# Performance work log

Measured on AMD Instinct MI355X. Metric: run time of the kernel, lower is better.

## Reference

```python
import jax, jax.numpy as jnp
import numpy as np

EPS = 0.1        # entropic regularization (init eps)
MAX_ITER = 100   # init max_iter
THRESH = 0.1     # early-stop threshold from original code
NORM_EPS = 1e-8


def setup_inputs() -> dict:
    key = jax.random.key(0)
    kx, ky = jax.random.split(key)
    x = jax.random.normal(kx, (16, 1024, 256), dtype=jnp.float32)
    y = jax.random.normal(ky, (16, 1024, 256), dtype=jnp.float32)
    return {"x": x, "y": y}


def _mfa_cost(x, y):
    # Cosine cost: E = 1 - cos(x_i, y_j), computed via normalized matmul
    # (norms clamped at 1e-8 as in torch CosineSimilarity).
    xn = x / jnp.maximum(jnp.linalg.norm(x, axis=-1, keepdims=True), NORM_EPS)
    yn = y / jnp.maximum(jnp.linalg.norm(y, axis=-1, keepdims=True), NORM_EPS)
    E = 1.0 - jnp.einsum('bnd,bmd->bnm', xn, yn)  # [B, N, M]

    B, N, M = E.shape
    log_mu = jnp.full((B, N), jnp.log(1.0 / N + 1e-8), dtype=E.dtype)
    log_nu = jnp.full((B, M), jnp.log(1.0 / M + 1e-8), dtype=E.dtype)

    def Mmat(u, v):
        # (-E + u_i + v_j) / eps, broadcast over [B, N, M]
        return (-E + u[..., :, None] + v[..., None, :]) / EPS

    @jax.checkpoint
    def body(carry, _):
        u, v, done = carry
        u_new = EPS * (log_mu - jax.nn.logsumexp(Mmat(u, v), axis=-1)) + u
        # original transposes then logsumexp over -1 == logsumexp over -2
        v_new = EPS * (log_nu - jax.nn.logsumexp(Mmat(u_new, v), axis=-2)) + v
        err = jnp.abs(u_new - u).sum(-1).mean()
        # emulate data-dependent break: freeze u, v once converged
        u_out = jnp.where(done, u, u_new)
        v_out = jnp.where(done, v, v_new)
        return (u_out, v_out, done | (err < THRESH)), None

    u0 = jnp.zeros((B, N), dtype=E.dtype)
    v0 = jnp.zeros((B, M), dtype=E.dtype)
    (u, v, _), _ = jax.lax.scan(body, (u0, v0, jnp.array(False)), None, length=MAX_ITER)

    pi = jnp.exp(Mmat(u, v))                 # transport plan [B, N, M]
    cost = jnp.sum(pi * E, axis=(-2, -1))    # [B]  (reduction='none')
    return cost


def reference(x, y):
    return _mfa_cost(x, y)
```

## Files before the change

### kernel.cpp

```cpp
#include <hip/hip_runtime.h>

typedef _Float16 half_t;
typedef __attribute__((ext_vector_type(8))) _Float16 half8;
typedef __attribute__((ext_vector_type(4))) float f32x4;
typedef __attribute__((ext_vector_type(8))) short short8v;
typedef unsigned short u16;
typedef unsigned int u32;

#define SCALE_F     14.4269504f
#define INV_SCALE_F 0.0693147181f
#define C_MU       -9.99998523f
#define C_NU       -9.99998523f
#define MU_F        0.000976572498f
#define ERR_STOP_B  1.44269504f
#define MAX_ITER    100
#define SPIN_LIMIT  50000000LL
#define PV0         3.0517578125e-05f

#define SMEM_E   131072
#define SMEM_CP  16384
#define SMEM_PV  4096
#define SMEM_RED 256
#define SMEM_TOTAL (SMEM_E + SMEM_CP + SMEM_PV + SMEM_RED)

#define PSTRIDE  520
#define NFLAGS   2048

__device__ __forceinline__ float fexp2(float x) { return __builtin_amdgcn_exp2f(x); }
__device__ __forceinline__ float flog2(float x) { return __builtin_amdgcn_logf(x); }
__device__ __forceinline__ float frcp(float x)  { return __builtin_amdgcn_rcpf(x); }

__device__ __forceinline__ u16 f2bf(float f) {
  unsigned u = __float_as_uint(f);
  return (u16)((u + 0x7fffu + ((u >> 16) & 1u)) >> 16);
}
__device__ __forceinline__ float bf2f(u16 h) {
  return __uint_as_float(((unsigned)h) << 16);
}
__device__ __forceinline__ u32 agload(const u32* p) {
  return __hip_atomic_load(p, __ATOMIC_RELAXED, __HIP_MEMORY_SCOPE_AGENT);
}
__device__ __forceinline__ void agstore(u32* p, u32 v) {
  __hip_atomic_store(p, v, __ATOMIC_RELAXED, __HIP_MEMORY_SCOPE_AGENT);
}
__device__ __forceinline__ int agload_i(const int* p) {
  return __hip_atomic_load(p, __ATOMIC_RELAXED, __HIP_MEMORY_SCOPE_AGENT);
}
__device__ __forceinline__ void agstore_i(int* p, int v) {
  __hip_atomic_store(p, v, __ATOMIC_RELAXED, __HIP_MEMORY_SCOPE_AGENT);
}

__global__ __launch_bounds__(256) void mfa_prep(const float* __restrict__ x,
                                                const float* __restrict__ y,
                                                u16* __restrict__ Xn,
                                                u16* __restrict__ Yn,
                                                int* __restrict__ flags,
                                                float* __restrict__ cost) {
  int g = blockIdx.x * 256 + threadIdx.x;
  if (g < NFLAGS) flags[g] = 0;
  if (g < 16) cost[g] = 0.0f;

  int wid = g >> 6;
  int lane = threadIdx.x & 63;
  for (int rr = 0; rr < 32; ++rr) {
    int row = wid + (rr << 10);
    const float* src = (row < 16384) ? x + (size_t)row * 256
                                     : y + (size_t)(row - 16384) * 256;
    float4 xa = ((const float4*)src)[lane];
    float ss = xa.x*xa.x + xa.y*xa.y + xa.z*xa.z + xa.w*xa.w;
    #pragma unroll
    for (int off = 32; off; off >>= 1) ss += __shfl_xor(ss, off);
    float inv = 1.0f / fmaxf(sqrtf(ss), 1e-8f);
    ushort4 o;
    o.x = f2bf(xa.x * inv); o.y = f2bf(xa.y * inv);
    o.z = f2bf(xa.z * inv); o.w = f2bf(xa.w * inv);
    u16* dst = ((row < 16384) ? Xn + ((size_t)row << 8)
                              : Yn + ((size_t)(row - 16384) << 8)) + lane * 4;
    *(ushort4*)dst = o;
  }
}

__global__ __launch_bounds__(512, 1) void mfa_sink_fused(
    const u16* __restrict__ Xn, const u16* __restrict__ Yn,
    u32* __restrict__ partials, int* __restrict__ flags,
    float* __restrict__ cost) {
  extern __shared__ char smem[];
  half_t* pEls = (half_t*)smem;
  float*  cpb  = (float*)(smem + SMEM_E);
  float*  pvsh = (float*)(smem + SMEM_E + SMEM_CP);
  float*  sred = (float*)(smem + SMEM_E + SMEM_CP + SMEM_PV);

  const int t = threadIdx.x, w = t >> 6, lane = t & 63;
  const int lane15 = lane & 15, lgrp = lane >> 4;
  const int blk = blockIdx.x;
  const int b = ((blk & 7) << 1) | ((blk >> 7) & 1);
  const int k = (blk >> 3) & 15;
  const int idx = (w << 6) + lane;

  {
    const u16* Xb = Xn + ((size_t)((b << 10) + (k << 6)) << 8);
    const u16* Yb = Yn + ((size_t)(b << 10) << 8);
    const int wcol = w << 7;
    #pragma unroll
    for (int pass = 0; pass < 2; ++pass) {
      const int c0 = wcol + (pass << 6);
      f32x4 acc[4][4];
      #pragma unroll
      for (int i = 0; i < 4; ++i)
        #pragma unroll
        for (int j = 0; j < 4; ++j) acc[i][j] = (f32x4){0.f, 0.f, 0.f, 0.f};
      for (int ks = 0; ks < 8; ++ks) {
        const int koff = (ks << 5) + (lgrp << 3);
        short8v a[4], bb[4];
        #pragma unroll
        for (int i = 0; i < 4; ++i)
          a[i] = *(const short8v*)(Xb + (((i << 4) + lane15) << 8) + koff);
        #pragma unroll
        for (int j = 0; j < 4; ++j)
          bb[j] = *(const short8v*)(Yb + ((size_t)(c0 + (j << 4) + lane15) << 8) + koff);
        #pragma unroll
        for (int i = 0; i < 4; ++i)
          #pragma unroll
          for (int j = 0; j < 4; ++j)
            acc[i][j] = __builtin_amdgcn_mfma_f32_16x16x32_bf16(a[i], bb[j], acc[i][j], 0, 0, 0);
      }
      #pragma unroll
      for (int i = 0; i < 4; ++i)
        #pragma unroll
        for (int j = 0; j < 4; ++j) {
          const int col = c0 + (j << 4) + lane15;
          #pragma unroll
          for (int q = 0; q < 4; ++q) {
            const int row = (i << 4) + (lgrp << 2) + q;
            pEls[(row << 10) + col] =
                (half_t)fexp2(15.0f - (1.0f - acc[i][j][q]) * SCALE_F);
          }
        }
    }
  }
  pvsh[t] = PV0; pvsh[t + 512] = PV0;
  __syncthreads();

  float ureg[8];
  #pragma unroll
  for (int r = 0; r < 8; ++r) ureg[r] = 0.0f;
  float vr0 = 0.0f, vr1 = 0.0f;

  const int mlo = lane << 3;
  int it = 0;
  for (; it < MAX_ITER; ++it) {
    const f32x4* p4 = (const f32x4*)pvsh;
    f32x4 a4 = p4[lane*2], b4 = p4[lane*2 + 1];
    f32x4 c4 = p4[128 + lane*2], d4 = p4[128 + lane*2 + 1];
    float pv[16];
    pv[0]=a4.x; pv[1]=a4.y; pv[2]=a4.z; pv[3]=a4.w;
    pv[4]=b4.x; pv[5]=b4.y; pv[6]=b4.z; pv[7]=b4.w;
    pv[8]=c4.x; pv[9]=c4.y; pv[10]=c4.z; pv[11]=c4.w;
    pv[12]=d4.x; pv[13]=d4.y; pv[14]=d4.z; pv[15]=d4.w;

    float inner[16];
    #pragma unroll
    for (int j = 0; j < 16; ++j) inner[j] = 0.0f;
    float werr = 0.0f;

    #pragma unroll
    for (int r = 0; r < 8; ++r) {
      const half8* E8 = (const half8*)(pEls + (((w << 3) + r) << 10));
      half8 ea = E8[lane], eb = E8[lane + 64];
      float pe[16];
      #pragma unroll
      for (int j = 0; j < 8; ++j) pe[j] = (float)ea[j];
      #pragma unroll
      for (int j = 0; j < 8; ++j) pe[8 + j] = (float)eb[j];
      float s = 0.0f;
      #pragma unroll
      for (int j = 0; j < 16; ++j) s = __builtin_fmaf(pv[j], pe[j], s);
      #pragma unroll
      for (int off = 32; off; off >>= 1) s += __shfl_xor(s, off);
      float unew = C_MU - flog2(s);
      float eu = MU_F * frcp(s);
      werr += fabsf(unew - ureg[r]);
      ureg[r] = unew;
      #pragma unroll
      for (int j = 0; j < 16; ++j) inner[j] = __builtin_fmaf(pe[j], eu, inner[j]);
    }
    float colacc[16];
    #pragma unroll
    for (int j = 0; j < 16; ++j) colacc[j] = inner[j] * pv[j];
    if (lane == 0) sred[w] = werr;

    if (w < 4) {
      #pragma unroll
      for (int j = 0; j < 4; ++j) {
        *(f32x4*)&cpb[w*1024 + mlo + 4*j - ((j>=2)?8:0) + ((j>=2)?512:0)] =
            (f32x4){colacc[4*j], colacc[4*j+1], colacc[4*j+2], colacc[4*j+3]};
      }
    }
    __syncthreads();
    if (w >= 4) {
      const int wb = (w - 4) * 1024;
      #pragma unroll
      for (int j = 0; j < 8; ++j) cpb[wb + mlo + j] += colacc[j];
      #pragma unroll
      for (int j = 0; j < 8; ++j) cpb[wb + 512 + mlo + j] += colacc[8 + j];
    }
    __syncthreads();

    const int p = it & 1;
    u32* ps = partials + (size_t)((((p << 4) | b) << 4) | k) * PSTRIDE;
    {
      const int c0 = idx << 1;
      float2 q0 = *(const float2*)&cpb[c0];
      float2 q1 = *(const float2*)&cpb[1024 + c0];
      float2 q2 = *(const float2*)&cpb[2048 + c0];
      float2 q3 = *(const float2*)&cpb[3072 + c0];
      float fa  = q0.x + q1.x + q2.x + q3.x;
      float fbv = q0.y + q1.y + q2.y + q3.y;
      agstore(&ps[idx], (u32)f2bf(fa) | ((u32)f2bf(fbv) << 16));
      if (t == 0) {
        float be = sred[0]+sred[1]+sred[2]+sred[3]+sred[4]+sred[5]+sred[6]+sred[7];
        agstore(&ps[512], __float_as_uint(be));
      }
    }
    asm volatile("s_waitcnt vmcnt(0)" ::: "memory");
    if (lane == 0)
      agstore_i(&flags[(b << 7) | (k << 3) | w], it + 1);

    {
      const int* fl = flags + (b << 7);
      const int tgt = it + 1;
      long long t0c = clock64();
      for (;;) {
        int f0 = agload_i(&fl[lane]);
        int f1 = agload_i(&fl[lane + 64]);
        if (__all((f0 >= tgt) && (f1 >= tgt))) break;
        if (clock64() - t0c > SPIN_LIMIT) break;
        __builtin_amdgcn_s_sleep(1);
      }
    }

    {
      const u32* pr = partials + (size_t)(((p << 4) | b) << 4) * PSTRIDE;
      u32 wv[16];
      #pragma unroll
      for (int j = 0; j < 16; ++j)
        wv[j] = agload(&pr[j * PSTRIDE + idx]);
      float t0s = 0.0f, t1s = 0.0f;
      #pragma unroll
      for (int j = 0; j < 16; ++j) {
        t0s += bf2f((u16)(wv[j] & 0xffffu));
        t1s += bf2f((u16)(wv[j] >> 16));
      }
      if (w == 0) {
        float we = 0.0f;
        if (lane < 16)
          we = __uint_as_float(agload(&pr[lane * PSTRIDE + 512]));
        #pragma unroll
        for (int off = 8; off; off >>= 1) we += __shfl_xor(we, off);
        if (lane == 0) sred[8] = we;
      }
      const int c0 = idx << 1;
      vr0 += C_NU - flog2(t0s);
      vr1 += C_NU - flog2(t1s);
      pvsh[c0]     = fexp2(vr0 - 15.0f);
      pvsh[c0 + 1] = fexp2(vr1 - 15.0f);
    }
    __syncthreads();

    if (sred[8] < ERR_STOP_B) break;
  }

  {
    const f32x4* p4 = (const f32x4*)pvsh;
    f32x4 a4 = p4[lane*2], b4 = p4[lane*2 + 1];
    f32x4 c4 = p4[128 + lane*2], d4 = p4[128 + lane*2 + 1];
    float pv[16];
    pv[0]=a4.x; pv[1]=a4.y; pv[2]=a4.z; pv[3]=a4.w;
    pv[4]=b4.x; pv[5]=b4.y; pv[6]=b4.z; pv[7]=b4.w;
    pv[8]=c4.x; pv[9]=c4.y; pv[10]=c4.z; pv[11]=c4.w;
    pv[12]=d4.x; pv[13]=d4.y; pv[14]=d4.z; pv[15]=d4.w;
    float cacc = 0.0f;
    #pragma unroll
    for (int r = 0; r < 8; ++r) {
      const half8* E8 = (const half8*)(pEls + (((w << 3) + r) << 10));
      half8 ea = E8[lane], eb = E8[lane + 64];
      float su = fexp2(ureg[r]);
      #pragma unroll
      for (int j = 0; j < 8; ++j) {
        float pe = (float)ea[j];
        float e = 15.0f - flog2(pe);
        cacc += su * pv[j] * pe * e;
      }
      #pragma unroll
      for (int j = 0; j < 8; ++j) {
        float pe = (float)eb[j];
        float e = 15.0f - flog2(pe);
        cacc += su * pv[8 + j] * pe * e;
      }
    }
    #pragma unroll
    for (int off = 32; off; off >>= 1) cacc += __shfl_xor(cacc, off);
    if (lane == 0) sred[w] = cacc;
    __syncthreads();
    if (t == 0)
      atomicAdd(&cost[b], (sred[0]+sred[1]+sred[2]+sred[3]+sred[4]+sred[5]+
                           sred[6]+sred[7]) * INV_SCALE_F);
  }
}

extern "C" void kernel_launch(void* const* d_in, const int* in_sizes, int n_in,
                              void* d_out, int out_size, void* d_ws, size_t ws_size,
                              hipStream_t stream) {
  const float* x = (const float*)d_in[0];
  const float* y = (const float*)d_in[1];
  float* cost = (float*)d_out;

  char* base = (char*)d_ws;
  u16* Xn       = (u16*)base;
  u16* Yn       = (u16*)(base + 8388608);
  u32* partials = (u32*)(base + 16777216);
  int* flags    = (int*)(base + 16777216 + (size_t)2*16*16*PSTRIDE*4);
  size_t needed = 16777216 + (size_t)2*16*16*PSTRIDE*4 + NFLAGS*4;
  if (ws_size < needed) return;

  mfa_prep<<<256, 256, 0, stream>>>(x, y, Xn, Yn, flags, cost);

  (void)hipFuncSetAttribute((const void*)mfa_sink_fused,
                            hipFuncAttributeMaxDynamicSharedMemorySize, SMEM_TOTAL);
  mfa_sink_fused<<<dim3(256), dim3(512), SMEM_TOTAL, stream>>>(
      Xn, Yn, partials, flags, cost);
}
```

Measured before the change: 87.19 us.

## Replace flag-based inter-block barrier with tagged partials and batch row reductions

Drops the separate per-wave flag array and its release/spin protocol. Each block now writes fp32 column partials whose two low mantissa bits carry an iteration tag, and readers spin on the partials themselves until every tag matches. This removes one store-wait-flag round trip per Sinkhorn iteration. The row pass is also split so all eight row dot-products are computed first and their cross-lane shuffles are batched, giving more instruction-level parallelism, at the cost of reading E from LDS twice. Partials double in size because they are now fp32 instead of bf16, the low-bit tagging slightly perturbs values, and the prep kernel must zero the whole partials buffer.

```diff
diff --git a/kernel.cpp b/kernel.cpp
--- a/kernel.cpp
+++ b/kernel.cpp
@@ -23,8 +23,8 @@
 #define SMEM_RED 256
 #define SMEM_TOTAL (SMEM_E + SMEM_CP + SMEM_PV + SMEM_RED)
 
-#define PSTRIDE  520
-#define NFLAGS   2048
+#define PSTRIDE  1040
+#define PWORDS   (2*16*16*PSTRIDE)
 
 __device__ __forceinline__ float fexp2(float x) { return __builtin_amdgcn_exp2f(x); }
 __device__ __forceinline__ float flog2(float x) { return __builtin_amdgcn_logf(x); }
@@ -34,19 +34,10 @@
   unsigned u = __float_as_uint(f);
   return (u16)((u + 0x7fffu + ((u >> 16) & 1u)) >> 16);
 }
-__device__ __forceinline__ float bf2f(u16 h) {
-  return __uint_as_float(((unsigned)h) << 16);
-}
 __device__ __forceinline__ u32 agload(const u32* p) {
   return __hip_atomic_load(p, __ATOMIC_RELAXED, __HIP_MEMORY_SCOPE_AGENT);
 }
 __device__ __forceinline__ void agstore(u32* p, u32 v) {
-  __hip_atomic_store(p, v, __ATOMIC_RELAXED, __HIP_MEMORY_SCOPE_AGENT);
-}
-__device__ __forceinline__ int agload_i(const int* p) {
-  return __hip_atomic_load(p, __ATOMIC_RELAXED, __HIP_MEMORY_SCOPE_AGENT);
-}
-__device__ __forceinline__ void agstore_i(int* p, int v) {
   __hip_atomic_store(p, v, __ATOMIC_RELAXED, __HIP_MEMORY_SCOPE_AGENT);
 }
 
@@ -54,11 +45,15 @@
                                                 const float* __restrict__ y,
                                                 u16* __restrict__ Xn,
                                                 u16* __restrict__ Yn,
-                                                int* __restrict__ flags,
+                                                u32* __restrict__ partials,
                                                 float* __restrict__ cost) {
   int g = blockIdx.x * 256 + threadIdx.x;
-  if (g < NFLAGS) flags[g] = 0;
   if (g < 16) cost[g] = 0.0f;
+  #pragma unroll
+  for (int j = 0; j < 9; ++j) {
+    int idx = (j << 16) + g;
+    if (idx < PWORDS) partials[idx] = 0u;
+  }
 
   int wid = g >> 6;
   int lane = threadIdx.x & 63;
@@ -82,8 +77,7 @@
 
 __global__ __launch_bounds__(512, 1) void mfa_sink_fused(
     const u16* __restrict__ Xn, const u16* __restrict__ Yn,
-    u32* __restrict__ partials, int* __restrict__ flags,
-    float* __restrict__ cost) {
+    u32* __restrict__ partials, float* __restrict__ cost) {
   extern __shared__ char smem[];
   half_t* pEls = (half_t*)smem;
   float*  cpb  = (float*)(smem + SMEM_E);
@@ -95,7 +89,6 @@
   const int blk = blockIdx.x;
   const int b = ((blk & 7) << 1) | ((blk >> 7) & 1);
   const int k = (blk >> 3) & 15;
-  const int idx = (w << 6) + lane;
 
   {
     const u16* Xb = Xn + ((size_t)((b << 10) + (k << 6)) << 8);
@@ -158,36 +151,47 @@
     pv[8]=c4.x; pv[9]=c4.y; pv[10]=c4.z; pv[11]=c4.w;
     pv[12]=d4.x; pv[13]=d4.y; pv[14]=d4.z; pv[15]=d4.w;
 
-    float inner[16];
-    #pragma unroll
-    for (int j = 0; j < 16; ++j) inner[j] = 0.0f;
-    float werr = 0.0f;
-
+    float s[8];
     #pragma unroll
     for (int r = 0; r < 8; ++r) {
       const half8* E8 = (const half8*)(pEls + (((w << 3) + r) << 10));
       half8 ea = E8[lane], eb = E8[lane + 64];
-      float pe[16];
-      #pragma unroll
-      for (int j = 0; j < 8; ++j) pe[j] = (float)ea[j];
-      #pragma unroll
-      for (int j = 0; j < 8; ++j) pe[8 + j] = (float)eb[j];
-      float s = 0.0f;
-      #pragma unroll
-      for (int j = 0; j < 16; ++j) s = __builtin_fmaf(pv[j], pe[j], s);
-      #pragma unroll
-      for (int off = 32; off; off >>= 1) s += __shfl_xor(s, off);
-      float unew = C_MU - flog2(s);
-      float eu = MU_F * frcp(s);
+      float acc = 0.0f;
+      #pragma unroll
+      for (int j = 0; j < 8; ++j) acc = __builtin_fmaf(pv[j], (float)ea[j], acc);
+      #pragma unroll
+      for (int j = 0; j < 8; ++j) acc = __builtin_fmaf(pv[8+j], (float)eb[j], acc);
+      s[r] = acc;
+    }
+    #pragma unroll
+    for (int off = 32; off; off >>= 1) {
+      #pragma unroll
+      for (int r = 0; r < 8; ++r) s[r] += __shfl_xor(s[r], off);
+    }
+    float eu[8], werr = 0.0f;
+    #pragma unroll
+    for (int r = 0; r < 8; ++r) {
+      float unew = C_MU - flog2(s[r]);
+      eu[r] = MU_F * frcp(s[r]);
       werr += fabsf(unew - ureg[r]);
       ureg[r] = unew;
-      #pragma unroll
-      for (int j = 0; j < 16; ++j) inner[j] = __builtin_fmaf(pe[j], eu, inner[j]);
+    }
+    if (lane == 0) sred[w] = werr;
+    float inner[16];
+    #pragma unroll
+    for (int j = 0; j < 16; ++j) inner[j] = 0.0f;
+    #pragma unroll
+    for (int r = 0; r < 8; ++r) {
+      const half8* E8 = (const half8*)(pEls + (((w << 3) + r) << 10));
+      half8 ea = E8[lane], eb = E8[lane + 64];
+      #pragma unroll
+      for (int j = 0; j < 8; ++j) inner[j] = __builtin_fmaf((float)ea[j], eu[r], inner[j]);
+      #pragma unroll
+      for (int j = 0; j < 8; ++j) inner[8+j] = __builtin_fmaf((float)eb[j], eu[r], inner[8+j]);
     }
     float colacc[16];
     #pragma unroll
     for (int j = 0; j < 16; ++j) colacc[j] = inner[j] * pv[j];
-    if (lane == 0) sred[w] = werr;
 
     if (w < 4) {
       #pragma unroll
@@ -207,63 +211,56 @@
     __syncthreads();
 
     const int p = it & 1;
-    u32* ps = partials + (size_t)((((p << 4) | b) << 4) | k) * PSTRIDE;
+    const u32 tag = (u32)((it + 1) & 3);
     {
-      const int c0 = idx << 1;
-      float2 q0 = *(const float2*)&cpb[c0];
-      float2 q1 = *(const float2*)&cpb[1024 + c0];
-      float2 q2 = *(const float2*)&cpb[2048 + c0];
-      float2 q3 = *(const float2*)&cpb[3072 + c0];
-      float fa  = q0.x + q1.x + q2.x + q3.x;
-      float fbv = q0.y + q1.y + q2.y + q3.y;
-      agstore(&ps[idx], (u32)f2bf(fa) | ((u32)f2bf(fbv) << 16));
+      u32* ps = partials + (size_t)((((p << 4) | b) << 4) | k) * PSTRIDE;
+      float fa = cpb[t] + cpb[1024 + t] + cpb[2048 + t] + cpb[3072 + t];
+      float fb = cpb[512 + t] + cpb[1536 + t] + cpb[2560 + t] + cpb[3584 + t];
+      agstore(&ps[t],       (__float_as_uint(fa) & ~3u) | tag);
+      agstore(&ps[512 + t], (__float_as_uint(fb) & ~3u) | tag);
       if (t == 0) {
         float be = sred[0]+sred[1]+sred[2]+sred[3]+sred[4]+sred[5]+sred[6]+sred[7];
-        agstore(&ps[512], __float_as_uint(be));
-      }
-    }
-    asm volatile("s_waitcnt vmcnt(0)" ::: "memory");
-    if (lane == 0)
-      agstore_i(&flags[(b << 7) | (k << 3) | w], it + 1);
-
-    {
-      const int* fl = flags + (b << 7);
-      const int tgt = it + 1;
-      long long t0c = clock64();
-      for (;;) {
-        int f0 = agload_i(&fl[lane]);
-        int f1 = agload_i(&fl[lane + 64]);
-        if (__all((f0 >= tgt) && (f1 >= tgt))) break;
-        if (clock64() - t0c > SPIN_LIMIT) break;
-        __builtin_amdgcn_s_sleep(1);
+        agstore(&ps[1024], (__float_as_uint(be) & ~3u) | tag);
       }
     }
 
     {
       const u32* pr = partials + (size_t)(((p << 4) | b) << 4) * PSTRIDE;
-      u32 wv[16];
-      #pragma unroll
-      for (int j = 0; j < 16; ++j)
-        wv[j] = agload(&pr[j * PSTRIDE + idx]);
+      u32 wa[16], wb[16], wwe = tag;
+      long long tws = clock64();
+      for (;;) {
+        #pragma unroll
+        for (int j = 0; j < 16; ++j) {
+          wa[j] = agload(&pr[j * PSTRIDE + t]);
+          wb[j] = agload(&pr[j * PSTRIDE + 512 + t]);
+        }
+        u32 diff = 0;
+        #pragma unroll
+        for (int j = 0; j < 16; ++j)
+          diff |= ((wa[j] ^ tag) | (wb[j] ^ tag)) & 3u;
+        if (w == 0 && lane < 16) {
+          wwe = agload(&pr[lane * PSTRIDE + 1024]);
+          diff |= (wwe ^ tag) & 3u;
+        }
+        if (__all(diff == 0)) break;
+        if (clock64() - tws > SPIN_LIMIT) break;
+      }
       float t0s = 0.0f, t1s = 0.0f;
       #pragma unroll
       for (int j = 0; j < 16; ++j) {
-        t0s += bf2f((u16)(wv[j] & 0xffffu));
-        t1s += bf2f((u16)(wv[j] >> 16));
+        t0s += __uint_as_float(wa[j] & ~3u);
+        t1s += __uint_as_float(wb[j] & ~3u);
       }
       if (w == 0) {
-        float we = 0.0f;
-        if (lane < 16)
-          we = __uint_as_float(agload(&pr[lane * PSTRIDE + 512]));
+        float we = __uint_as_float(wwe & ~3u);
         #pragma unroll
         for (int off = 8; off; off >>= 1) we += __shfl_xor(we, off);
         if (lane == 0) sred[8] = we;
       }
-      const int c0 = idx << 1;
       vr0 += C_NU - flog2(t0s);
       vr1 += C_NU - flog2(t1s);
-      pvsh[c0]     = fexp2(vr0 - 15.0f);
-      pvsh[c0 + 1] = fexp2(vr1 - 15.0f);
+      pvsh[t]       = fexp2(vr0 - 15.0f);
+      pvsh[t + 512] = fexp2(vr1 - 15.0f);
     }
     __syncthreads();
 
@@ -319,14 +316,13 @@
   u16* Xn       = (u16*)base;
   u16* Yn       = (u16*)(base + 8388608);
   u32* partials = (u32*)(base + 16777216);
-  int* flags    = (int*)(base + 16777216 + (size_t)2*16*16*PSTRIDE*4);
-  size_t needed = 16777216 + (size_t)2*16*16*PSTRIDE*4 + NFLAGS*4;
+  size_t needed = 16777216 + (size_t)PWORDS * 4;
   if (ws_size < needed) return;
 
-  mfa_prep<<<256, 256, 0, stream>>>(x, y, Xn, Yn, flags, cost);
+  mfa_prep<<<256, 256, 0, stream>>>(x, y, Xn, Yn, partials, cost);
 
   (void)hipFuncSetAttribute((const void*)mfa_sink_fused,
                             hipFuncAttributeMaxDynamicSharedMemorySize, SMEM_TOTAL);
   mfa_sink_fused<<<dim3(256), dim3(512), SMEM_TOTAL, stream>>>(
-      Xn, Yn, partials, flags, cost);
-}
+      Xn, Yn, partials, cost);
+}
```

Measured after the change: 74.71 us. 14.3% less time.
